# Optimization experiments

Hardware: AMD Instinct MI355X
Metric: run time of the kernel (lower is better)

The kernel has to match this reference:

```python
import jax, jax.numpy as jnp
import numpy as np

N = 100000   # nodes
E = 1600000  # edges (avg degree 16)
IN, H, OUT, P = 100, 256, 256, 128
EPS = 1e-5


def setup_inputs() -> dict:
    key = jax.random.key(0)
    ks = jax.random.split(key, 12)

    def lin(k, o, i):
        return jax.random.normal(k, (o, i), jnp.float32) / np.float32(np.sqrt(i))

    return {
        "x": jax.random.normal(ks[0], (N, IN), jnp.float32),
        "edge_index": jax.random.randint(ks[1], (2, E), 0, N),
        # SAGEConv l (aggregated-neighbor branch, has bias) and r (root branch, no bias)
        "Wl0": lin(ks[2], H, IN), "bl0": jnp.zeros((H,), jnp.float32), "Wr0": lin(ks[3], H, IN),
        "Wl1": lin(ks[4], H, H),  "bl1": jnp.zeros((H,), jnp.float32), "Wr1": lin(ks[5], H, H),
        "Wl2": lin(ks[6], OUT, H), "bl2": jnp.zeros((OUT,), jnp.float32), "Wr2": lin(ks[7], OUT, H),
        # projection head + BatchNorm1d(128)
        "Wp": lin(ks[8], P, OUT), "bp": jnp.zeros((P,), jnp.float32),
        "gamma": jnp.ones((P,), jnp.float32), "beta": jnp.zeros((P,), jnp.float32),
    }


def _sage_conv(x, src, dst, Wl, bl, Wr):
    # PyG SAGEConv default: mean-aggregate source features into destinations,
    # then lin_l(agg) + lin_r(x).
    agg = jax.ops.segment_sum(x[src], dst, num_segments=N)           # [N, d]
    deg = jax.ops.segment_sum(jnp.ones((src.shape[0],), x.dtype), dst, num_segments=N)
    agg = agg / jnp.maximum(deg, 1.0)[:, None]
    return agg @ Wl.T + bl + x @ Wr.T


def reference(x, edge_index, Wl0, bl0, Wr0, Wl1, bl1, Wr1, Wl2, bl2, Wr2, Wp, bp, gamma, beta):
    src, dst = edge_index[0], edge_index[1]
    x = jax.nn.relu(_sage_conv(x, src, dst, Wl0, bl0, Wr0))  # dropout is identity in eval
    x = jax.nn.relu(_sage_conv(x, src, dst, Wl1, bl1, Wr1))
    x = _sage_conv(x, src, dst, Wl2, bl2, Wr2)               # no relu on last layer
    z = x @ Wp.T + bp                                        # projection head -> [N, 128]
    mu = jnp.mean(z, axis=0)
    var = jnp.var(z, axis=0)                                 # biased, as torch BN uses for normalization
    h = gamma * (z - mu) * jax.lax.rsqrt(var + EPS) + beta
    return (x, h)
```

## Files before the change

kernel.cpp:

```cpp
#include <hip/hip_runtime.h>
#include <hip/hip_bf16.h>

#define EPS_BN 1e-5f

using short8  = __attribute__((ext_vector_type(8))) short;
using ushort8 = __attribute__((ext_vector_type(8))) unsigned short;
using f32x4   = __attribute__((ext_vector_type(4))) float;

__device__ inline float bf2f(unsigned short u) {
    union { unsigned i; float f; } c; c.i = ((unsigned)u) << 16; return c.f;
}
__device__ inline unsigned short f2bf(float f) {
    unsigned x = __float_as_uint(f);
    unsigned r = (x + 0x7FFF + ((x >> 16) & 1)) >> 16;
    return (unsigned short)r;
}

__global__ void zero_i32(int* __restrict__ p, int n) {
    int i = blockIdx.x * blockDim.x + threadIdx.x;
    if (i < n) p[i] = 0;
}
__global__ void zero_f32(float* __restrict__ p, int n) {
    int i = blockIdx.x * blockDim.x + threadIdx.x;
    if (i < n) p[i] = 0.0f;
}

__global__ void conv_w(const float* __restrict__ w, unsigned short* __restrict__ o,
                       int R, int C, int CP) {
    int t = blockIdx.x * blockDim.x + threadIdx.x;
    if (t >= R * CP) return;
    int r = t / CP, c = t % CP;
    o[t] = (c < C) ? f2bf(w[(size_t)r * C + c]) : (unsigned short)0;
}

__global__ void conv_x_pad(const float* __restrict__ x, unsigned short* __restrict__ xp, int n) {
    int t = blockIdx.x * blockDim.x + threadIdx.x;
    if (t >= n * 32) return;
    int node = t >> 5, g = t & 31;
    int f0 = g * 4;
    ushort4 o;
    const float* xr = x + (size_t)node * 100;
    o.x = (f0 + 0 < 100) ? f2bf(xr[f0 + 0]) : 0;
    o.y = (f0 + 1 < 100) ? f2bf(xr[f0 + 1]) : 0;
    o.z = (f0 + 2 < 100) ? f2bf(xr[f0 + 2]) : 0;
    o.w = (f0 + 3 < 100) ? f2bf(xr[f0 + 3]) : 0;
    *(ushort4*)(xp + (size_t)node * 128 + f0) = o;
}

__global__ void count_k(const int* __restrict__ dst, int* __restrict__ counts, int E) {
    int i = blockIdx.x * blockDim.x + threadIdx.x;
    if (i < E) atomicAdd(&counts[dst[i]], 1);
}

__global__ void scan1(const int* __restrict__ counts, int* __restrict__ rp,
                      int* __restrict__ partials, int n) {
    __shared__ int s[256];
    int t = threadIdx.x;
    int i = blockIdx.x * 256 + t;
    int v = (i < n) ? counts[i] : 0;
    s[t] = v;
    __syncthreads();
    for (int off = 1; off < 256; off <<= 1) {
        int u = (t >= off) ? s[t - off] : 0;
        __syncthreads();
        s[t] += u;
        __syncthreads();
    }
    if (i < n) rp[i] = s[t] - v;
    if (t == 255) partials[blockIdx.x] = s[255];
}

__global__ void scan2(int* __restrict__ partials, int nb) {
    __shared__ int s[512];
    int t = threadIdx.x;
    int v = (t < nb) ? partials[t] : 0;
    s[t] = v;
    __syncthreads();
    for (int off = 1; off < 512; off <<= 1) {
        int u = (t >= off) ? s[t - off] : 0;
        __syncthreads();
        s[t] += u;
        __syncthreads();
    }
    if (t < nb) partials[t] = s[t] - v;
}

__global__ void scan3(int* __restrict__ rp, const int* __restrict__ partials, int n, int E) {
    int i = blockIdx.x * blockDim.x + threadIdx.x;
    if (i < n) rp[i] += partials[i >> 8];
    if (i == 0) rp[n] = E;
}

__global__ void fill_k(const int* __restrict__ src, const int* __restrict__ dst,
                       const int* __restrict__ rp, int* __restrict__ cursor,
                       int* __restrict__ col, int E) {
    int i = blockIdx.x * blockDim.x + threadIdx.x;
    if (i < E) {
        int d = dst[i];
        int pos = atomicAdd(&cursor[d], 1);
        col[rp[d] + pos] = src[i];
    }
}

__global__ __launch_bounds__(256) void agg_bf16_256(
    const unsigned short* __restrict__ x, const int* __restrict__ rp,
    const int* __restrict__ col, unsigned short* __restrict__ out, int n) {
    int wave = threadIdx.x >> 6, lane = threadIdx.x & 63;
    int node = blockIdx.x * 4 + wave;
    if (node >= n) return;
    int s = rp[node], e = rp[node + 1];
    int deg = e - s;
    int h = lane >> 5;
    int l32 = lane & 31;

    float a[8] = {0, 0, 0, 0, 0, 0, 0, 0};
    int base = 0;
    for (; base + 8 <= deg; base += 8) {
        int i = s + base + h;
        int r0 = col[i], r1 = col[i + 2], r2 = col[i + 4], r3 = col[i + 6];
        ushort8 v0 = *(const ushort8*)(x + (size_t)r0 * 256 + l32 * 8);
        ushort8 v1 = *(const ushort8*)(x + (size_t)r1 * 256 + l32 * 8);
        ushort8 v2 = *(const ushort8*)(x + (size_t)r2 * 256 + l32 * 8);
        ushort8 v3 = *(const ushort8*)(x + (size_t)r3 * 256 + l32 * 8);
#pragma unroll
        for (int j = 0; j < 8; ++j)
            a[j] += bf2f(v0[j]) + bf2f(v1[j]) + bf2f(v2[j]) + bf2f(v3[j]);
    }
    for (int i = s + base + h; i < e; i += 2) {
        int r = col[i];
        ushort8 v = *(const ushort8*)(x + (size_t)r * 256 + l32 * 8);
#pragma unroll
        for (int j = 0; j < 8; ++j) a[j] += bf2f(v[j]);
    }
#pragma unroll
    for (int j = 0; j < 8; ++j) a[j] += __shfl_xor(a[j], 32);

    if (h == 0) {
        float sc = 1.0f / fmaxf((float)deg, 1.0f);
        ushort8 o;
#pragma unroll
        for (int j = 0; j < 8; ++j) o[j] = f2bf(a[j] * sc);
        *(ushort8*)(out + (size_t)node * 256 + l32 * 8) = o;
    }
}

__global__ __launch_bounds__(256) void agg_bf16_128(
    const unsigned short* __restrict__ x, const int* __restrict__ rp,
    const int* __restrict__ col, unsigned short* __restrict__ out, int n) {
    int wave = threadIdx.x >> 6, lane = threadIdx.x & 63;
    int node = blockIdx.x * 4 + wave;
    if (node >= n) return;
    int s = rp[node], e = rp[node + 1];
    int deg = e - s;
    int q = lane >> 4;
    int l16 = lane & 15;

    float a[8] = {0, 0, 0, 0, 0, 0, 0, 0};
    int base = 0;
    for (; base + 16 <= deg; base += 16) {
        int i = s + base + q;
        int r0 = col[i], r1 = col[i + 4], r2 = col[i + 8], r3 = col[i + 12];
        ushort8 v0 = *(const ushort8*)(x + (size_t)r0 * 128 + l16 * 8);
        ushort8 v1 = *(const ushort8*)(x + (size_t)r1 * 128 + l16 * 8);
        ushort8 v2 = *(const ushort8*)(x + (size_t)r2 * 128 + l16 * 8);
        ushort8 v3 = *(const ushort8*)(x + (size_t)r3 * 128 + l16 * 8);
#pragma unroll
        for (int j = 0; j < 8; ++j)
            a[j] += bf2f(v0[j]) + bf2f(v1[j]) + bf2f(v2[j]) + bf2f(v3[j]);
    }
    for (int i = s + base + q; i < e; i += 4) {
        int r = col[i];
        ushort8 v = *(const ushort8*)(x + (size_t)r * 128 + l16 * 8);
#pragma unroll
        for (int j = 0; j < 8; ++j) a[j] += bf2f(v[j]);
    }
#pragma unroll
    for (int j = 0; j < 8; ++j) {
        a[j] += __shfl_xor(a[j], 16);
        a[j] += __shfl_xor(a[j], 32);
    }

    if (lane < 16) {
        float sc = 1.0f / fmaxf((float)deg, 1.0f);
        ushort8 o;
#pragma unroll
        for (int j = 0; j < 8; ++j) o[j] = f2bf(a[j] * sc);
        *(ushort8*)(out + (size_t)node * 128 + l16 * 8) = o;
    }
}

template <int KTOT, int DOUT, bool HAS_AGG, bool RELU, bool STF32, bool STBF16, int WAVES_M>
__global__ __launch_bounds__(512) void sage_mfma(
    const unsigned short* __restrict__ xp, const unsigned short* __restrict__ ap,
    const unsigned short* __restrict__ Wr, const unsigned short* __restrict__ Wl,
    const float* __restrict__ bias,
    float* __restrict__ outf, unsigned short* __restrict__ outb, int n) {
    constexpr int WAVES_N = 8 / WAVES_M;
    constexpr int KS = KTOT / 32;
    static_assert(DOUT / 16 / WAVES_N == 4, "wave owns 4 col tiles");

    const int t = threadIdx.x;
    const int wave = t >> 6, lane = t & 63;
    const int wm = wave / WAVES_N, wn = wave % WAVES_N;
    const int lcol = lane & 15, lq = lane >> 4;
    const int node_base = blockIdx.x * (WAVES_M * 64) + wm * 64;
    const int col0 = wn * 64;

    f32x4 acc[4][4];
#pragma unroll
    for (int ct = 0; ct < 4; ++ct) {
        float b = bias[col0 + ct * 16 + lcol];
#pragma unroll
        for (int mt = 0; mt < 4; ++mt) {
            acc[mt][ct][0] = b; acc[mt][ct][1] = b; acc[mt][ct][2] = b; acc[mt][ct][3] = b;
        }
    }

    const unsigned short* aPx[4];
    const unsigned short* aPa[4];
    const unsigned short* bPr[4];
    const unsigned short* bPl[4];
#pragma unroll
    for (int i = 0; i < 4; ++i) {
        aPx[i] = xp + (size_t)(node_base + i * 16 + lcol) * KTOT + lq * 8;
        bPr[i] = Wr + (size_t)(col0 + i * 16 + lcol) * KTOT + lq * 8;
        if (HAS_AGG) {
            aPa[i] = ap + (size_t)(node_base + i * 16 + lcol) * KTOT + lq * 8;
            bPl[i] = Wl + (size_t)(col0 + i * 16 + lcol) * KTOT + lq * 8;
        }
    }

    short8 axE[4], aaE[4], brE[4], blE[4];
    short8 axO[4], aaO[4], brO[4], blO[4];

    auto LOAD = [&](int ks, short8 (&ax)[4], short8 (&aa)[4],
                    short8 (&br)[4], short8 (&bl)[4]) {
#pragma unroll
        for (int i = 0; i < 4; ++i) {
            ax[i] = *(const short8*)(aPx[i] + ks * 32);
            br[i] = *(const short8*)(bPr[i] + ks * 32);
        }
        if constexpr (HAS_AGG) {
#pragma unroll
            for (int i = 0; i < 4; ++i) {
                aa[i] = *(const short8*)(aPa[i] + ks * 32);
                bl[i] = *(const short8*)(bPl[i] + ks * 32);
            }
        }
    };
    auto MM = [&](short8 (&ax)[4], short8 (&aa)[4],
                  short8 (&br)[4], short8 (&bl)[4]) {
#pragma unroll
        for (int mt = 0; mt < 4; ++mt)
#pragma unroll
            for (int ct = 0; ct < 4; ++ct) {
                acc[mt][ct] = __builtin_amdgcn_mfma_f32_16x16x32_bf16(
                    ax[mt], br[ct], acc[mt][ct], 0, 0, 0);
                if constexpr (HAS_AGG)
                    acc[mt][ct] = __builtin_amdgcn_mfma_f32_16x16x32_bf16(
                        aa[mt], bl[ct], acc[mt][ct], 0, 0, 0);
            }
    };

    LOAD(0, axE, aaE, brE, blE);
#pragma unroll
    for (int ks = 0; ks < KS; ks += 2) {
        LOAD(ks + 1, axO, aaO, brO, blO);
        MM(axE, aaE, brE, blE);
        if (ks + 2 < KS) LOAD(ks + 2, axE, aaE, brE, blE);
        MM(axO, aaO, brO, blO);
    }

#pragma unroll
    for (int mt = 0; mt < 4; ++mt) {
        int nb0 = node_base + mt * 16;
        if (nb0 >= n) continue;
#pragma unroll
        for (int ct = 0; ct < 4; ++ct) {
            f32x4 v = acc[mt][ct];
            if (RELU) {
                v[0] = fmaxf(v[0], 0.0f); v[1] = fmaxf(v[1], 0.0f);
                v[2] = fmaxf(v[2], 0.0f); v[3] = fmaxf(v[3], 0.0f);
            }
            int colI = col0 + ct * 16 + lcol;
#pragma unroll
            for (int j = 0; j < 4; ++j) {
                size_t row = (size_t)nb0 + lq * 4 + j;
                if (STF32) outf[row * DOUT + colI] = v[j];
                if (STBF16) outb[row * DOUT + colI] = f2bf(v[j]);
            }
        }
    }
}

__global__ void bn_partial(const float* __restrict__ z, float* __restrict__ sums, int n) {
    int f = threadIdx.x & 127;
    int half = threadIdx.x >> 7;
    float s = 0.0f, s2 = 0.0f;
    for (int row = blockIdx.x * 2 + half; row < n; row += gridDim.x * 2) {
        float v = z[(size_t)row * 128 + f];
        s += v; s2 += v * v;
    }
    __shared__ float ls[256], ls2[256];
    ls[threadIdx.x] = s; ls2[threadIdx.x] = s2;
    __syncthreads();
    if (half == 0) {
        atomicAdd(&sums[f], s + ls[128 + f]);
        atomicAdd(&sums[128 + f], s2 + ls2[128 + f]);
    }
}

__global__ void bn_finalize(const float* __restrict__ sums, const float* __restrict__ gamma,
                            const float* __restrict__ beta, float* __restrict__ params, int n) {
    int f = threadIdx.x;
    float mu = sums[f] / (float)n;
    float var = sums[128 + f] / (float)n - mu * mu;
    float inv = rsqrtf(var + EPS_BN);
    float sc = gamma[f] * inv;
    params[f] = sc;
    params[128 + f] = beta[f] - mu * sc;
}

__global__ void bn_apply(float* __restrict__ z, const float* __restrict__ params, int total4) {
    int i = blockIdx.x * blockDim.x + threadIdx.x;
    for (; i < total4; i += gridDim.x * blockDim.x) {
        float4 v = ((float4*)z)[i];
        int f0 = (i & 31) * 4;
        v.x = v.x * params[f0 + 0] + params[128 + f0 + 0];
        v.y = v.y * params[f0 + 1] + params[128 + f0 + 1];
        v.z = v.z * params[f0 + 2] + params[128 + f0 + 2];
        v.w = v.w * params[f0 + 3] + params[128 + f0 + 3];
        ((float4*)z)[i] = v;
    }
}

extern "C" void kernel_launch(void* const* d_in, const int* in_sizes, int n_in,
                              void* d_out, int out_size, void* d_ws, size_t ws_size,
                              hipStream_t stream) {
    const float* x_in  = (const float*)d_in[0];
    const int*   ei    = (const int*)d_in[1];
    const float* Wl0   = (const float*)d_in[2];
    const float* bl0   = (const float*)d_in[3];
    const float* Wr0   = (const float*)d_in[4];
    const float* Wl1   = (const float*)d_in[5];
    const float* bl1   = (const float*)d_in[6];
    const float* Wr1   = (const float*)d_in[7];
    const float* Wl2   = (const float*)d_in[8];
    const float* bl2   = (const float*)d_in[9];
    const float* Wr2   = (const float*)d_in[10];
    const float* Wp    = (const float*)d_in[11];
    const float* bp    = (const float*)d_in[12];
    const float* gamma = (const float*)d_in[13];
    const float* beta  = (const float*)d_in[14];

    const int IN = 100, INP = 128, H = 256, OUT = 256, P = 128;
    const int n = in_sizes[0] / IN;
    const int E = in_sizes[1] / 2;
    const int* src = ei;
    const int* dst = ei + E;

    size_t off = 0;
    auto alloc = [&](size_t bytes) -> char* {
        char* p = (char*)d_ws + off;
        off += (bytes + 255) & ~(size_t)255;
        return p;
    };
    int*   counts   = (int*)alloc((size_t)n * 4);
    int*   cursor   = (int*)alloc((size_t)n * 4);
    int*   rp       = (int*)alloc((size_t)(n + 1) * 4);
    int*   partials = (int*)alloc(512 * 4);
    int*   col      = (int*)alloc((size_t)E * 4);
    unsigned short* Wl0b = (unsigned short*)alloc((size_t)H * INP * 2);
    unsigned short* Wr0b = (unsigned short*)alloc((size_t)H * INP * 2);
    unsigned short* Wl1b = (unsigned short*)alloc((size_t)H * H * 2);
    unsigned short* Wr1b = (unsigned short*)alloc((size_t)H * H * 2);
    unsigned short* Wl2b = (unsigned short*)alloc((size_t)OUT * H * 2);
    unsigned short* Wr2b = (unsigned short*)alloc((size_t)OUT * H * 2);
    unsigned short* Wpb  = (unsigned short*)alloc((size_t)P * OUT * 2);
    float* bnsums   = (float*)alloc(256 * 4);
    float* bnparams = (float*)alloc(256 * 4);
    unsigned short* bufA = (unsigned short*)alloc((size_t)n * H * 2);
    unsigned short* bufB = (unsigned short*)alloc((size_t)n * H * 2);
    unsigned short* bufC = (unsigned short*)alloc((size_t)n * H * 2);
    unsigned short* bufD = (unsigned short*)alloc((size_t)n * H * 2);
    (void)alloc((size_t)256 * 512);

    unsigned short* xpad   = bufA;
    unsigned short* aggpad = bufA + (size_t)n * INP;
    unsigned short* h1b  = bufB;
    unsigned short* agg1 = bufC;
    unsigned short* h2b  = bufD;
    unsigned short* agg2 = bufB;
    unsigned short* xb2  = bufA;

    float* out_x = (float*)d_out;
    float* z     = out_x + (size_t)n * OUT;

    const int nb = (n + 255) / 256;

    zero_i32<<<nb, 256, 0, stream>>>(counts, n);
    zero_i32<<<nb, 256, 0, stream>>>(cursor, n);
    zero_f32<<<1, 256, 0, stream>>>(bnsums, 256);
    count_k<<<(E + 255) / 256, 256, 0, stream>>>(dst, counts, E);
    scan1<<<nb, 256, 0, stream>>>(counts, rp, partials, n);
    scan2<<<1, 512, 0, stream>>>(partials, nb);
    scan3<<<nb, 256, 0, stream>>>(rp, partials, n, E);
    fill_k<<<(E + 255) / 256, 256, 0, stream>>>(src, dst, rp, cursor, col, E);

    conv_x_pad<<<(n * 32 + 255) / 256, 256, 0, stream>>>(x_in, xpad, n);
    conv_w<<<(H * INP + 255) / 256, 256, 0, stream>>>(Wl0, Wl0b, H, IN, INP);
    conv_w<<<(H * INP + 255) / 256, 256, 0, stream>>>(Wr0, Wr0b, H, IN, INP);
    conv_w<<<(H * H + 255) / 256, 256, 0, stream>>>(Wl1, Wl1b, H, H, H);
    conv_w<<<(H * H + 255) / 256, 256, 0, stream>>>(Wr1, Wr1b, H, H, H);
    conv_w<<<(OUT * H + 255) / 256, 256, 0, stream>>>(Wl2, Wl2b, OUT, H, H);
    conv_w<<<(OUT * H + 255) / 256, 256, 0, stream>>>(Wr2, Wr2b, OUT, H, H);
    conv_w<<<(P * OUT + 255) / 256, 256, 0, stream>>>(Wp, Wpb, P, OUT, OUT);

    agg_bf16_128<<<(n + 3) / 4, 256, 0, stream>>>(xpad, rp, col, aggpad, n);
    sage_mfma<128, 256, true, true, false, true, 2><<<(n + 127) / 128, 512, 0, stream>>>(
        xpad, aggpad, Wr0b, Wl0b, bl0, nullptr, h1b, n);

    agg_bf16_256<<<(n + 3) / 4, 256, 0, stream>>>(h1b, rp, col, agg1, n);
    sage_mfma<256, 256, true, true, false, true, 2><<<(n + 127) / 128, 512, 0, stream>>>(
        h1b, agg1, Wr1b, Wl1b, bl1, nullptr, h2b, n);

    agg_bf16_256<<<(n + 3) / 4, 256, 0, stream>>>(h2b, rp, col, agg2, n);
    sage_mfma<256, 256, true, false, true, true, 2><<<(n + 127) / 128, 512, 0, stream>>>(
        h2b, agg2, Wr2b, Wl2b, bl2, out_x, xb2, n);

    sage_mfma<256, 128, false, false, true, false, 4><<<(n + 255) / 256, 512, 0, stream>>>(
        xb2, nullptr, Wpb, nullptr, bp, z, nullptr, n);

    bn_partial<<<256, 256, 0, stream>>>(z, bnsums, n);
    bn_finalize<<<1, 128, 0, stream>>>(bnsums, gamma, beta, bnparams, n);
    bn_apply<<<2048, 256, 0, stream>>>(z, bnparams, n * (P / 4));
}
```

Baseline: 912.9 us.

## Stage GEMM operand tiles in LDS via direct global-to-LDS loads

Rewrites the fused SAGE GEMM kernel so that A (node features and aggregates) and B (weights) k-slices are loaded cooperatively into shared memory with global_load_lds, then read by all waves. Before, each wave loaded its operands directly into registers. Blocks now cover 128 nodes × 128 output columns with 4 waves, using a 2D grid over node and column tiles. This is meant to cut redundant global loads through reuse across waves, but it adds two barriers per k-step and drops the register double-buffering, so load latency is no longer hidden.

```diff
diff --git a/kernel.cpp b/kernel.cpp
--- a/kernel.cpp
+++ b/kernel.cpp
@@ -6,6 +6,9 @@
 using short8  = __attribute__((ext_vector_type(8))) short;
 using ushort8 = __attribute__((ext_vector_type(8))) unsigned short;
 using f32x4   = __attribute__((ext_vector_type(4))) float;
+
+typedef const __attribute__((address_space(1))) void* gas_ptr;
+typedef __attribute__((address_space(3))) void* las_ptr;
 
 __device__ inline float bf2f(unsigned short u) {
     union { unsigned i; float f; } c; c.i = ((unsigned)u) << 16; return c.f;
@@ -189,92 +192,80 @@
     }
 }
 
-template <int KTOT, int DOUT, bool HAS_AGG, bool RELU, bool STF32, bool STBF16, int WAVES_M>
-__global__ __launch_bounds__(512) void sage_mfma(
+template <int KTOT, int DOUT, bool HAS_AGG, bool RELU, bool STF32, bool STBF16>
+__global__ __launch_bounds__(256) void sage_mfma(
     const unsigned short* __restrict__ xp, const unsigned short* __restrict__ ap,
     const unsigned short* __restrict__ Wr, const unsigned short* __restrict__ Wl,
     const float* __restrict__ bias,
     float* __restrict__ outf, unsigned short* __restrict__ outb, int n) {
-    constexpr int WAVES_N = 8 / WAVES_M;
+    constexpr int NSRC = HAS_AGG ? 2 : 1;
+    constexpr int NCHUNK = NSRC * 16;
+    constexpr int CPW = NCHUNK / 4;
     constexpr int KS = KTOT / 32;
-    static_assert(DOUT / 16 / WAVES_N == 4, "wave owns 4 col tiles");
+    __shared__ __align__(16) unsigned short lds[NCHUNK * 512];
 
     const int t = threadIdx.x;
     const int wave = t >> 6, lane = t & 63;
-    const int wm = wave / WAVES_N, wn = wave % WAVES_N;
+    const int wm = wave >> 1, wn = wave & 1;
     const int lcol = lane & 15, lq = lane >> 4;
-    const int node_base = blockIdx.x * (WAVES_M * 64) + wm * 64;
-    const int col0 = wn * 64;
+    const int node_base = blockIdx.x * 128;
+    const int col_base = blockIdx.y * 128;
+
+    const int p_w = HAS_AGG ? wave : (wave >> 1);
+    const int tile0 = HAS_AGG ? 0 : (wave & 1) * 4;
+    const unsigned short* gpan;
+    int growbase;
+    if constexpr (HAS_AGG) {
+        gpan = (p_w == 0) ? xp : (p_w == 1) ? ap : (p_w == 2) ? Wr : Wl;
+        growbase = (p_w < 2) ? node_base : col_base;
+    } else {
+        gpan = (p_w == 0) ? xp : Wr;
+        growbase = (p_w == 0) ? node_base : col_base;
+    }
+    const unsigned short* gbase =
+        gpan + (size_t)(growbase + tile0 * 16 + lcol) * KTOT + lq * 8;
+    const int cbase = (p_w * 8 + tile0) * 512;
 
     f32x4 acc[4][4];
 #pragma unroll
     for (int ct = 0; ct < 4; ++ct) {
-        float b = bias[col0 + ct * 16 + lcol];
+        float b = bias[col_base + wn * 64 + ct * 16 + lcol];
 #pragma unroll
         for (int mt = 0; mt < 4; ++mt) {
             acc[mt][ct][0] = b; acc[mt][ct][1] = b; acc[mt][ct][2] = b; acc[mt][ct][3] = b;
         }
     }
 
-    const unsigned short* aPx[4];
-    const unsigned short* aPa[4];
-    const unsigned short* bPr[4];
-    const unsigned short* bPl[4];
-#pragma unroll
-    for (int i = 0; i < 4; ++i) {
-        aPx[i] = xp + (size_t)(node_base + i * 16 + lcol) * KTOT + lq * 8;
-        bPr[i] = Wr + (size_t)(col0 + i * 16 + lcol) * KTOT + lq * 8;
-        if (HAS_AGG) {
-            aPa[i] = ap + (size_t)(node_base + i * 16 + lcol) * KTOT + lq * 8;
-            bPl[i] = Wl + (size_t)(col0 + i * 16 + lcol) * KTOT + lq * 8;
+    for (int ks = 0; ks < KS; ++ks) {
+#pragma unroll
+        for (int i = 0; i < CPW; ++i) {
+            const unsigned short* g = gbase + (size_t)i * 16 * KTOT + ks * 32;
+            __builtin_amdgcn_global_load_lds((gas_ptr)g, (las_ptr)(lds + cbase + i * 512),
+                                             16, 0, 0);
         }
-    }
-
-    short8 axE[4], aaE[4], brE[4], blE[4];
-    short8 axO[4], aaO[4], brO[4], blO[4];
-
-    auto LOAD = [&](int ks, short8 (&ax)[4], short8 (&aa)[4],
-                    short8 (&br)[4], short8 (&bl)[4]) {
-#pragma unroll
-        for (int i = 0; i < 4; ++i) {
-            ax[i] = *(const short8*)(aPx[i] + ks * 32);
-            br[i] = *(const short8*)(bPr[i] + ks * 32);
+        __syncthreads();
+#pragma unroll
+        for (int s = 0; s < NSRC; ++s) {
+            short8 af[4], bf[4];
+#pragma unroll
+            for (int i = 0; i < 4; ++i) {
+                af[i] = *(const short8*)(lds + (s * 8 + wm * 4 + i) * 512 + lane * 8);
+                bf[i] = *(const short8*)(lds + ((NSRC + s) * 8 + wn * 4 + i) * 512 + lane * 8);
+            }
+#pragma unroll
+            for (int mt = 0; mt < 4; ++mt)
+#pragma unroll
+                for (int ct = 0; ct < 4; ++ct)
+                    acc[mt][ct] = __builtin_amdgcn_mfma_f32_16x16x32_bf16(
+                        af[mt], bf[ct], acc[mt][ct], 0, 0, 0);
         }
-        if constexpr (HAS_AGG) {
-#pragma unroll
-            for (int i = 0; i < 4; ++i) {
-                aa[i] = *(const short8*)(aPa[i] + ks * 32);
-                bl[i] = *(const short8*)(bPl[i] + ks * 32);
-            }
-        }
-    };
-    auto MM = [&](short8 (&ax)[4], short8 (&aa)[4],
-                  short8 (&br)[4], short8 (&bl)[4]) {
-#pragma unroll
-        for (int mt = 0; mt < 4; ++mt)
-#pragma unroll
-            for (int ct = 0; ct < 4; ++ct) {
-                acc[mt][ct] = __builtin_amdgcn_mfma_f32_16x16x32_bf16(
-                    ax[mt], br[ct], acc[mt][ct], 0, 0, 0);
-                if constexpr (HAS_AGG)
-                    acc[mt][ct] = __builtin_amdgcn_mfma_f32_16x16x32_bf16(
-                        aa[mt], bl[ct], acc[mt][ct], 0, 0, 0);
-            }
-    };
-
-    LOAD(0, axE, aaE, brE, blE);
-#pragma unroll
-    for (int ks = 0; ks < KS; ks += 2) {
-        LOAD(ks + 1, axO, aaO, brO, blO);
-        MM(axE, aaE, brE, blE);
-        if (ks + 2 < KS) LOAD(ks + 2, axE, aaE, brE, blE);
-        MM(axO, aaO, brO, blO);
+        __syncthreads();
     }
 
 #pragma unroll
     for (int mt = 0; mt < 4; ++mt) {
-        int nb0 = node_base + mt * 16;
-        if (nb0 >= n) continue;
+        int row0 = node_base + wm * 64 + mt * 16 + lq * 4;
+        if (row0 >= n) continue;
 #pragma unroll
         for (int ct = 0; ct < 4; ++ct) {
             f32x4 v = acc[mt][ct];
@@ -282,12 +273,14 @@
                 v[0] = fmaxf(v[0], 0.0f); v[1] = fmaxf(v[1], 0.0f);
                 v[2] = fmaxf(v[2], 0.0f); v[3] = fmaxf(v[3], 0.0f);
             }
-            int colI = col0 + ct * 16 + lcol;
+            int colI = col_base + wn * 64 + ct * 16 + lcol;
 #pragma unroll
             for (int j = 0; j < 4; ++j) {
-                size_t row = (size_t)nb0 + lq * 4 + j;
-                if (STF32) outf[row * DOUT + colI] = v[j];
-                if (STBF16) outb[row * DOUT + colI] = f2bf(v[j]);
+                int row = row0 + j;
+                if (row < n) {
+                    if (STF32) outf[(size_t)row * DOUT + colI] = v[j];
+                    if (STBF16) outb[(size_t)row * DOUT + colI] = f2bf(v[j]);
+                }
             }
         }
     }
@@ -397,6 +390,7 @@
     float* z     = out_x + (size_t)n * OUT;
 
     const int nb = (n + 255) / 256;
+    const int gx = (n + 127) / 128;
 
     zero_i32<<<nb, 256, 0, stream>>>(counts, n);
     zero_i32<<<nb, 256, 0, stream>>>(cursor, n);
@@ -417,18 +411,18 @@
     conv_w<<<(P * OUT + 255) / 256, 256, 0, stream>>>(Wp, Wpb, P, OUT, OUT);
 
     agg_bf16_128<<<(n + 3) / 4, 256, 0, stream>>>(xpad, rp, col, aggpad, n);
-    sage_mfma<128, 256, true, true, false, true, 2><<<(n + 127) / 128, 512, 0, stream>>>(
+    sage_mfma<128, 256, true, true, false, true><<<dim3(gx, 2), 256, 0, stream>>>(
         xpad, aggpad, Wr0b, Wl0b, bl0, nullptr, h1b, n);
 
     agg_bf16_256<<<(n + 3) / 4, 256, 0, stream>>>(h1b, rp, col, agg1, n);
-    sage_mfma<256, 256, true, true, false, true, 2><<<(n + 127) / 128, 512, 0, stream>>>(
+    sage_mfma<256, 256, true, true, false, true><<<dim3(gx, 2), 256, 0, stream>>>(
         h1b, agg1, Wr1b, Wl1b, bl1, nullptr, h2b, n);
 
     agg_bf16_256<<<(n + 3) / 4, 256, 0, stream>>>(h2b, rp, col, agg2, n);
-    sage_mfma<256, 256, true, false, true, true, 2><<<(n + 127) / 128, 512, 0, stream>>>(
+    sage_mfma<256, 256, true, false, true, true><<<dim3(gx, 2), 256, 0, stream>>>(
         h2b, agg2, Wr2b, Wl2b, bl2, out_x, xb2, n);
 
-    sage_mfma<256, 128, false, false, true, false, 4><<<(n + 255) / 256, 512, 0, stream>>>(
+    sage_mfma<256, 128, false, false, true, false><<<dim3(gx, 1), 256, 0, stream>>>(
         xb2, nullptr, Wpb, nullptr, bp, z, nullptr, n);
 
     bn_partial<<<256, 256, 0, stream>>>(z, bnsums, n);
```

After: 767.0 us. -16.0%, faster.
